# Kernel tuning notes

Measured on AMD Instinct MI355X. Metric: run time of the kernel, lower is better.

## Reference

```python
import jax, jax.numpy as jnp
import numpy as np

# H2RConfig constants
KERNEL = 3
MAX_ROUTES = 1000
STRIDE = 4.0
MIN_SIZE = 32.0
MAX_SIZE = 512.0
SCORE_POWER = 2.0
UNC_WEIGHT = 0.35


def setup_inputs() -> dict:
    key = jax.random.key(0)
    k1, k2, k3 = jax.random.split(key, 3)
    shape = (32, 1, 512, 512)  # [B, 1, H, W] heatmaps at stride 4
    return {
        "route_logits": jax.random.normal(k1, shape, jnp.float32),
        "scale_logits": jax.random.normal(k2, shape, jnp.float32),
        "uncertainty_logits": jax.random.normal(k3, shape, jnp.float32),
        "image_h": 2048,
        "image_w": 2048,
    }


def reference(route_logits, scale_logits, uncertainty_logits, image_h, image_w):
    # score map: sigmoid^power, modulated by uncertainty (use_route_uncertainty=True)
    score = jnp.power(jax.nn.sigmoid(route_logits), SCORE_POWER)
    score = score * (1.0 - UNC_WEIGHT * jax.nn.sigmoid(uncertainty_logits))

    # local-max NMS: 3x3 max pool, stride 1, SAME padding (torch pads with -inf)
    pooled = jax.lax.reduce_window(
        score, -jnp.inf, jax.lax.max,
        window_dimensions=(1, 1, KERNEL, KERNEL),
        window_strides=(1, 1, 1, 1),
        padding="SAME",
    )
    peak_mask = score == pooled
    filtered = jnp.where(peak_mask, score, -1.0)

    B = score.shape[0]
    Wd = score.shape[3]
    flat = filtered.reshape(B, -1)                 # [B, H*W]
    values, indices = jax.lax.top_k(flat, MAX_ROUTES)  # [B, K]
    valid = values > 0.0                            # torch drops these; we mask/pad

    ys = indices // Wd
    xs = indices % Wd
    cx = (xs.astype(jnp.float32) + 0.5) * STRIDE
    cy = (ys.astype(jnp.float32) + 0.5) * STRIDE

    # gather scale / uncertainty at peak locations
    sc = jnp.take_along_axis(scale_logits.reshape(B, -1), indices, axis=1)
    un = jax.nn.sigmoid(jnp.take_along_axis(uncertainty_logits.reshape(B, -1), indices, axis=1))

    side = MIN_SIZE + jax.nn.sigmoid(sc) * (MAX_SIZE - MIN_SIZE)
    side = side * (1.0 + 0.25 * un)
    half = side * 0.5

    iw = float(image_w)
    ih = float(image_h)
    x1 = jnp.clip(cx - half, 0.0, iw - 1.0)
    y1 = jnp.clip(cy - half, 0.0, ih - 1.0)
    x2 = jnp.clip(cx + half, 1.0, iw)
    y2 = jnp.clip(cy + half, 1.0, ih)

    bcol = jnp.broadcast_to(jnp.arange(B, dtype=jnp.float32)[:, None], values.shape)
    rois = jnp.stack([bcol, x1, y1, x2, y2], axis=-1)  # [B, K, 5]

    # padded (fixed-shape) equivalent of torch's variable-length concat
    rois = jnp.where(valid[..., None], rois, 0.0)
    scores = jnp.where(valid, values, 0.0)
    return rois, scores, valid
```

## Files before the change

kernel.cpp:

```cpp
#include <hip/hip_runtime.h>
#include <hip/hip_bf16.h>
#include <math.h>


#define B_   32
#define H_   512
#define W_   512
#define HW_  (H_ * W_)
#define K_   1000
#define ROWS_ 16
#define THR_  512
#define NSTRIP_ 32
#define NBUK_ 4096
#define GCAP_ 2048
#define HSEG_ 128
#define NSEGB_ (NSTRIP_ * 8)
#define HOTBITS_ 0x3F000000u
#define WBASE_ (NBUK_ - 64)
#define FBCAP_ 45056

#define HL_BYTES_  ((size_t)B_ * NSEGB_ * HSEG_ * 8)
#define GW_BYTES_  ((size_t)B_ * NSTRIP_ * 64 * 4)
#define HC_BYTES_  ((size_t)B_ * NSEGB_ * 4)

__device__ __forceinline__ float np_expf(float x) {
#pragma clang fp contract(off)
    const float log2e = 1.44269504088896341f;
    float z = x * log2e;
    float m = rintf(z);
    float r = fmaf(m, -0.693359375f, x);
    r = fmaf(m, 2.12194440e-4f, r);
    float r2 = r * r;
    float p = fmaf(1.9875691500e-4f, r, 1.3981999507e-3f);
    p = fmaf(p, r, 8.3334519073e-3f);
    p = fmaf(p, r, 4.1665795894e-2f);
    p = fmaf(p, r, 1.6666665459e-1f);
    p = fmaf(p, r, 5.0000001201e-1f);
    p = fmaf(p, r2, r);
    p = p + 1.0f;
    int mi = (int)m;
    float sc = __int_as_float((127 + mi) << 23);
    return p * sc;
}

__device__ __forceinline__ float sigmoid_np(float x) {
#pragma clang fp contract(off)
    float e = np_expf(-x);
    float d = 1.0f + e;
    return 1.0f / d;
}

__device__ __forceinline__ float score_ref(float r, float u) {
#pragma clang fp contract(off)
    float s  = sigmoid_np(r);
    float s2 = s * s;
    float su = sigmoid_np(u);
    float t  = 0.35f * su;
    float m  = 1.0f - t;
    return s2 * m;
}

__device__ __forceinline__ float sigmoid_fast(float x) {
    return 1.0f / (1.0f + __expf(-x));
}

__global__ __launch_bounds__(THR_, 4) void fused_peak_kernel(
    const float* __restrict__ route, const float* __restrict__ unc,
    unsigned long long* __restrict__ hotlist,
    unsigned int* __restrict__ ghw,
    int* __restrict__ hcnt8)
{
    __shared__ float sm[ROWS_ + 2][W_];
    __shared__ unsigned int whist[64];

    const int tid   = threadIdx.x;
    const int lane  = tid & 63;
    const int wid   = tid >> 6;
    const int strip = blockIdx.x;
    const int b     = blockIdx.y;
    const int r0    = strip * ROWS_;
    if (tid < 64) whist[tid] = 0u;

    const float4* rb4 = (const float4*)(route + (size_t)b * HW_);
    const float4* ub4 = (const float4*)(unc   + (size_t)b * HW_);
    unsigned long long* hseg =
        hotlist + ((size_t)(b * NSTRIP_ + strip) * 8 + wid) * HSEG_;

    float4 rv[5], uv[5];
    int lrow[5], c4[5]; bool ok[5];
    #pragma unroll
    for (int k = 0; k < 5; ++k) {
        int slot = tid + k * THR_;
        slot = slot < 2303 ? slot : 2303;
        int row = slot >> 7;
        int gy  = r0 - 1 + row;
        lrow[k] = row; c4[k] = slot & 127;
        ok[k]   = (gy >= 0 && gy < H_);
        int cy  = gy < 0 ? 0 : (gy >= H_ ? H_ - 1 : gy);
        rv[k] = rb4[cy * 128 + c4[k]];
        uv[k] = ub4[cy * 128 + c4[k]];
    }
    #pragma unroll
    for (int k = 0; k < 5; ++k) {
        float4 s;
        s.x = score_ref(rv[k].x, uv[k].x);
        s.y = score_ref(rv[k].y, uv[k].y);
        s.z = score_ref(rv[k].z, uv[k].z);
        s.w = score_ref(rv[k].w, uv[k].w);
        if (!ok[k]) { s.x = -INFINITY; s.y = -INFINITY;
                      s.z = -INFINITY; s.w = -INFINITY; }
        *(float4*)&sm[lrow[k]][c4[k] * 4] = s;
    }
    __syncthreads();

    const unsigned long long lt = (1ull << lane) - 1ull;
    int wn = 0;
    #pragma unroll
    for (int j = 0; j < 4; ++j) {
        int g  = tid + j * THR_;
        int ly = 1 + (g >> 7);
        int x0 = (g & 127) * 4;
        int gy = r0 + (ly - 1);
        float4 q0 = *(const float4*)&sm[ly - 1][x0];
        float4 q1 = *(const float4*)&sm[ly    ][x0];
        float4 q2 = *(const float4*)&sm[ly + 1][x0];
        bool hasL = (x0 > 0), hasR = (x0 + 4 < W_);
        float l0 = hasL ? sm[ly - 1][x0 - 1] : -INFINITY;
        float l1 = hasL ? sm[ly    ][x0 - 1] : -INFINITY;
        float l2 = hasL ? sm[ly + 1][x0 - 1] : -INFINITY;
        float e0 = hasR ? sm[ly - 1][x0 + 4] : -INFINITY;
        float e1 = hasR ? sm[ly    ][x0 + 4] : -INFINITY;
        float e2 = hasR ? sm[ly + 1][x0 + 4] : -INFINITY;
        float f_m1 = fmaxf(l0, fmaxf(l1, l2));
        float f_0  = fmaxf(q0.x, fmaxf(q1.x, q2.x));
        float f_1  = fmaxf(q0.y, fmaxf(q1.y, q2.y));
        float f_2  = fmaxf(q0.z, fmaxf(q1.z, q2.z));
        float f_3  = fmaxf(q0.w, fmaxf(q1.w, q2.w));
        float f_4  = fmaxf(e0, fmaxf(e1, e2));
        float tb0  = fmaxf(q0.x, q2.x);
        float tb1  = fmaxf(q0.y, q2.y);
        float tb2  = fmaxf(q0.z, q2.z);
        float tb3  = fmaxf(q0.w, q2.w);
        float vv[4] = { q1.x, q1.y, q1.z, q1.w };
        float mm[4];
        mm[0] = fmaxf(fmaxf(f_m1, f_1), tb0);
        mm[1] = fmaxf(fmaxf(f_0,  f_2), tb1);
        mm[2] = fmaxf(fmaxf(f_1,  f_3), tb2);
        mm[3] = fmaxf(fmaxf(f_2,  f_4), tb3);
        #pragma unroll
        for (int i = 0; i < 4; ++i) {
            bool take = (vv[i] >= mm[i]);
            unsigned int bits = __float_as_uint(vv[i]);
            bool hot = take && (bits >= HOTBITS_);
            unsigned long long hmk = __ballot(hot);
            if (hot) {
                int hp = wn + __popcll(hmk & lt);
                if (hp < HSEG_) {
                    unsigned int idx = (unsigned int)(gy * W_ + x0 + i);
                    hseg[hp] = ((unsigned long long)bits << 32)
                               | (0xFFFFFFFFu - idx);
                    atomicAdd(&whist[(bits >> 18) - WBASE_], 1u);
                }
            }
            wn += __popcll(hmk);
        }
    }
    __syncthreads();

    if (lane == 0)
        hcnt8[(b * NSTRIP_ + strip) * 8 + wid] = wn < HSEG_ ? wn : HSEG_;
    if (tid < 64)
        ghw[(size_t)(b * NSTRIP_ + strip) * 64 + tid] = whist[tid];
}

__global__ __launch_bounds__(1024) void select2_kernel(
    const float* __restrict__ route, const float* __restrict__ unc_r,
    const float* __restrict__ scale, const float* __restrict__ unc,
    const unsigned long long* __restrict__ hotlist,
    const unsigned int* __restrict__ ghw,
    const int* __restrict__ hcnt8,
    unsigned long long* __restrict__ fbbuf,
    const int* __restrict__ ih_p, const int* __restrict__ iw_p,
    float* __restrict__ out)
{
    __shared__ __align__(16) unsigned char u_[(ROWS_ + 2) * W_ * 4];
    __shared__ unsigned int hist[NBUK_];
    __shared__ int sh_T, sh_nc, sh_fb, sh_fn;

    float (*sm)[W_] = (float (*)[W_])u_;
    unsigned int* cursor = (unsigned int*)u_;
    unsigned long long* grp = (unsigned long long*)(u_ + 16384);

    const int b = blockIdx.x, tid = threadIdx.x;
    const int lane = tid & 63, wid = tid >> 6;

    if (tid == 0) { sh_fb = 0; sh_T = 1; sh_nc = 0; sh_fn = 0; }
    if (tid < 64) hist[WBASE_ + tid] = 0u;
    __syncthreads();
    {
        const unsigned int* gw = ghw + (size_t)b * NSTRIP_ * 64;
        for (int i = tid; i < NSTRIP_ * 64; i += 1024) {
            unsigned int v = gw[i];
            if (v) atomicAdd(&hist[WBASE_ + (i & 63)], v);
        }
    }
    __syncthreads();

    if (wid == 0) {
        int cnt = (int)hist[WBASE_ + lane];
        int sum = cnt;
        #pragma unroll
        for (int off = 32; off > 0; off >>= 1)
            sum += __shfl_down(sum, off, 64);
        sum = __shfl(sum, 0, 64);
        if (sum < K_) {
            if (lane == 0) sh_fb = 1;
        } else {
            int suf = cnt;
            #pragma unroll
            for (int off = 1; off < 64; off <<= 1) {
                int o = __shfl_down(suf, off, 64);
                suf += (lane + off < 64) ? o : 0;
            }
            bool cond = suf >= K_;
            unsigned long long mask = __ballot(cond);
            int ls = 63 - __builtin_clzll(mask);
            if (lane >= ls) cursor[WBASE_ + lane] = (unsigned int)(suf - cnt);
            int ncv = __shfl(suf, ls, 64);
            if (lane == 0) { sh_T = WBASE_ + ls; sh_nc = ncv; }
        }
    }
    __syncthreads();
    const int fb = sh_fb;

    if (fb) {
        for (int i = tid; i < NBUK_; i += 1024) hist[i] = 0u;
        __syncthreads();

        const float4* rb4 = (const float4*)(route + (size_t)b * HW_);
        const float4* ub4 = (const float4*)(unc_r + (size_t)b * HW_);
        unsigned long long* fbb = fbbuf + (size_t)b * FBCAP_;

        for (int strip = 0; strip < NSTRIP_; ++strip) {
            const int r0 = strip * ROWS_;
            __syncthreads();
            for (int slot = tid; slot < 2304; slot += 1024) {
                int row = slot >> 7;
                int gy  = r0 - 1 + row;
                int c4  = slot & 127;
                bool okr = (gy >= 0 && gy < H_);
                int cy  = gy < 0 ? 0 : (gy >= H_ ? H_ - 1 : gy);
                float4 r4 = rb4[cy * 128 + c4];
                float4 u4 = ub4[cy * 128 + c4];
                float4 s;
                s.x = score_ref(r4.x, u4.x);
                s.y = score_ref(r4.y, u4.y);
                s.z = score_ref(r4.z, u4.z);
                s.w = score_ref(r4.w, u4.w);
                if (!okr) { s.x = -INFINITY; s.y = -INFINITY;
                            s.z = -INFINITY; s.w = -INFINITY; }
                *(float4*)&sm[row][c4 * 4] = s;
            }
            __syncthreads();
            for (int g = tid; g < 2048; g += 1024) {
                int ly = 1 + (g >> 7);
                int x0 = (g & 127) * 4;
                int gy = r0 + (ly - 1);
                float4 q0 = *(const float4*)&sm[ly - 1][x0];
                float4 q1 = *(const float4*)&sm[ly    ][x0];
                float4 q2 = *(const float4*)&sm[ly + 1][x0];
                bool hasL = (x0 > 0), hasR = (x0 + 4 < W_);
                float l0 = hasL ? sm[ly - 1][x0 - 1] : -INFINITY;
                float l1 = hasL ? sm[ly    ][x0 - 1] : -INFINITY;
                float l2 = hasL ? sm[ly + 1][x0 - 1] : -INFINITY;
                float e0 = hasR ? sm[ly - 1][x0 + 4] : -INFINITY;
                float e1 = hasR ? sm[ly    ][x0 + 4] : -INFINITY;
                float e2 = hasR ? sm[ly + 1][x0 + 4] : -INFINITY;
                float f_m1 = fmaxf(l0, fmaxf(l1, l2));
                float f_0  = fmaxf(q0.x, fmaxf(q1.x, q2.x));
                float f_1  = fmaxf(q0.y, fmaxf(q1.y, q2.y));
                float f_2  = fmaxf(q0.z, fmaxf(q1.z, q2.z));
                float f_3  = fmaxf(q0.w, fmaxf(q1.w, q2.w));
                float f_4  = fmaxf(e0, fmaxf(e1, e2));
                float tb0  = fmaxf(q0.x, q2.x);
                float tb1  = fmaxf(q0.y, q2.y);
                float tb2  = fmaxf(q0.z, q2.z);
                float tb3  = fmaxf(q0.w, q2.w);
                float vv[4] = { q1.x, q1.y, q1.z, q1.w };
                float mm[4];
                mm[0] = fmaxf(fmaxf(f_m1, f_1), tb0);
                mm[1] = fmaxf(fmaxf(f_0,  f_2), tb1);
                mm[2] = fmaxf(fmaxf(f_1,  f_3), tb2);
                mm[3] = fmaxf(fmaxf(f_2,  f_4), tb3);
                #pragma unroll
                for (int i = 0; i < 4; ++i) {
                    if (vv[i] >= mm[i]) {
                        unsigned int bits = __float_as_uint(vv[i]);
                        unsigned int idx  = (unsigned int)(gy * W_ + x0 + i);
                        int p = atomicAdd(&sh_fn, 1);
                        if (p < FBCAP_) {
                            fbb[p] = ((unsigned long long)bits << 32)
                                     | (0xFFFFFFFFu - idx);
                            atomicAdd(&hist[bits >> 18], 1u);
                        }
                    }
                }
            }
        }
        __syncthreads();

        if (wid == 0) {
            int Tv = 0;
            int total = 0;
            for (int c = NBUK_ / 64 - 1; c >= 0; --c) {
                int cnt = (int)hist[c * 64 + lane];
                int sum = cnt;
                #pragma unroll
                for (int off = 32; off > 0; off >>= 1)
                    sum += __shfl_down(sum, off, 64);
                sum = __shfl(sum, 0, 64);
                if (total + sum < K_) { total += sum; continue; }
                int suf = cnt;
                #pragma unroll
                for (int off = 1; off < 64; off <<= 1) {
                    int o = __shfl_down(suf, off, 64);
                    suf += (lane + off < 64) ? o : 0;
                }
                bool cond = (total + suf) >= K_;
                unsigned long long mask = __ballot(cond);
                int ls = 63 - __builtin_clzll(mask);
                Tv = c * 64 + ls;
                break;
            }
            if (Tv < 1) Tv = 1;
            int run = 0;
            for (int cb = NBUK_ - 64; cb >= (Tv & ~63); cb -= 64) {
                int beta = cb + lane;
                int cnt = (beta >= Tv) ? (int)hist[beta] : 0;
                int suf = cnt;
                #pragma unroll
                for (int off = 1; off < 64; off <<= 1) {
                    int o = __shfl_down(suf, off, 64);
                    suf += (lane + off < 64) ? o : 0;
                }
                int chunk_total = __shfl(suf, 0, 64);
                if (beta >= Tv) cursor[beta] = (unsigned int)(run + (suf - cnt));
                run += chunk_total;
            }
            if (lane == 0) { sh_T = Tv; sh_nc = run; }
        }
    }
    __syncthreads();
    const unsigned int T = (unsigned int)sh_T;

    if (!fb) {
        const unsigned long long* hb = hotlist + (size_t)b * NSEGB_ * HSEG_;
        const int* hc = hcnt8 + b * NSEGB_;
        for (int s = wid; s < NSEGB_; s += 16) {
            int c = hc[s];
            const unsigned long long* hs = hb + (size_t)s * HSEG_;
            for (int base = 0; base < c; base += 64) {
                int i = base + lane;
                unsigned long long key = (i < c) ? hs[i] : 0ull;
                unsigned int bk = (unsigned int)(key >> 50);
                if (bk >= T) {
                    unsigned int pos = atomicAdd(&cursor[bk], 1u);
                    if (pos < GCAP_) grp[pos] = key;
                }
            }
        }
    } else {
        const unsigned long long* fbb = fbbuf + (size_t)b * FBCAP_;
        int n = sh_fn; if (n > FBCAP_) n = FBCAP_;
        for (int i = tid; i < n; i += 1024) {
            unsigned long long k = fbb[i];
            unsigned int b0 = (unsigned int)(k >> 50);
            if (b0 >= T) {
                unsigned int pos = atomicAdd(&cursor[b0], 1u);
                if (pos < GCAP_) grp[pos] = k;
            }
        }
    }
    __syncthreads();

    const float fih = (float)(*ih_p);
    const float fiw = (float)(*iw_p);
    float* rois   = out;
    float* scores = out + (size_t)B_ * K_ * 5;
    float* validf = out + (size_t)B_ * K_ * 6;

    int nc = sh_nc;
    int ncEff = nc < GCAP_ ? nc : GCAP_;
    for (int p = tid; p < ncEff; p += 1024) {
        unsigned long long key = grp[p];
        unsigned int beta = (unsigned int)(key >> 50);
        int segEnd   = (int)cursor[beta];
        int segStart = segEnd - (int)hist[beta];
        int qEnd = segEnd < GCAP_ ? segEnd : GCAP_;
        int r = 0;
        for (int q = segStart; q < qEnd; ++q)
            r += (grp[q] > key) ? 1 : 0;
        int rank = segStart + r;
        if (rank < K_) {
            int o = b * K_ + rank;
            unsigned int bits = (unsigned int)(key >> 32);
            float v = __uint_as_float(bits);
            unsigned int idx = 0xFFFFFFFFu - (unsigned int)(key & 0xFFFFFFFFull);
            int y = (int)(idx >> 9), x = (int)(idx & 511u);
            float cx = ((float)x + 0.5f) * 4.0f;
            float cy = ((float)y + 0.5f) * 4.0f;
            float ss = sigmoid_fast(scale[(size_t)b * HW_ + idx]);
            float su = sigmoid_fast(unc  [(size_t)b * HW_ + idx]);
            float side = (32.0f + ss * 480.0f) * (1.0f + 0.25f * su);
            float half = 0.5f * side;
            float x1 = fminf(fmaxf(cx - half, 0.0f), fiw - 1.0f);
            float y1 = fminf(fmaxf(cy - half, 0.0f), fih - 1.0f);
            float x2 = fminf(fmaxf(cx + half, 1.0f), fiw);
            float y2 = fminf(fmaxf(cy + half, 1.0f), fih);
            rois[o * 5 + 0] = (float)b;
            rois[o * 5 + 1] = x1; rois[o * 5 + 2] = y1;
            rois[o * 5 + 3] = x2; rois[o * 5 + 4] = y2;
            scores[o] = v; validf[o] = 1.0f;
        }
    }
    for (int k = nc + tid; k < K_; k += 1024) {
        int o = b * K_ + k;
        rois[o * 5 + 0] = 0.0f; rois[o * 5 + 1] = 0.0f;
        rois[o * 5 + 2] = 0.0f; rois[o * 5 + 3] = 0.0f;
        rois[o * 5 + 4] = 0.0f;
        scores[o] = 0.0f; validf[o] = 0.0f;
    }
}

extern "C" void kernel_launch(void* const* d_in, const int* in_sizes, int n_in,
                              void* d_out, int out_size, void* d_ws, size_t ws_size,
                              hipStream_t stream) {
    const float* route = (const float*)d_in[0];
    const float* scale = (const float*)d_in[1];
    const float* unc   = (const float*)d_in[2];
    const int*   ih    = (const int*)d_in[3];
    const int*   iw    = (const int*)d_in[4];
    float* out = (float*)d_out;

    unsigned char* base = (unsigned char*)d_ws;
    unsigned long long* hotlist = (unsigned long long*)base;
    unsigned int* ghw = (unsigned int*)(base + HL_BYTES_);
    int* hcnt8        = (int*)(base + HL_BYTES_ + GW_BYTES_);
    unsigned long long* fbbuf =
        (unsigned long long*)(base + HL_BYTES_ + GW_BYTES_ + HC_BYTES_);

    dim3 g(NSTRIP_, B_);
    fused_peak_kernel<<<g, THR_, 0, stream>>>(route, unc, hotlist, ghw,
                                              hcnt8);
    select2_kernel<<<B_, 1024, 0, stream>>>(route, unc, scale, unc,
                                            hotlist, ghw, hcnt8, fbbuf,
                                            ih, iw, out);
}
```

Baseline: 172.7 us.

## Move hot-candidate histogram from peak kernel into selection kernel with finer buckets

Drops the per-block shared-memory histogram atomics, the trailing __syncthreads and the ghw global writes from the peak-finding kernel. The selection kernel now builds a finer 2048-bucket histogram (12-bit granularity above the hot threshold) directly from the hotlist entries, then finds the threshold bucket and scatters keys with cursors. This is meant to lighten the bandwidth-bound first kernel and shrink the tie groups in the rank step. The cost is that the single-block-per-batch select kernel reads the hotlist twice and does more work in its threshold scan.

New measurement: 167.6 us. 1.03x faster.

```diff
diff --git a/kernel.cpp b/kernel.cpp
--- a/kernel.cpp
+++ b/kernel.cpp
@@ -12,15 +12,14 @@
 #define THR_  512
 #define NSTRIP_ 32
 #define NBUK_ 4096
+#define NFB_  2048
 #define GCAP_ 2048
 #define HSEG_ 128
 #define NSEGB_ (NSTRIP_ * 8)
 #define HOTBITS_ 0x3F000000u
-#define WBASE_ (NBUK_ - 64)
 #define FBCAP_ 45056
 
 #define HL_BYTES_  ((size_t)B_ * NSEGB_ * HSEG_ * 8)
-#define GW_BYTES_  ((size_t)B_ * NSTRIP_ * 64 * 4)
 #define HC_BYTES_  ((size_t)B_ * NSEGB_ * 4)
 
 __device__ __forceinline__ float np_expf(float x) {
@@ -67,11 +66,9 @@
 __global__ __launch_bounds__(THR_, 4) void fused_peak_kernel(
     const float* __restrict__ route, const float* __restrict__ unc,
     unsigned long long* __restrict__ hotlist,
-    unsigned int* __restrict__ ghw,
     int* __restrict__ hcnt8)
 {
     __shared__ float sm[ROWS_ + 2][W_];
-    __shared__ unsigned int whist[64];
 
     const int tid   = threadIdx.x;
     const int lane  = tid & 63;
@@ -79,7 +76,6 @@
     const int strip = blockIdx.x;
     const int b     = blockIdx.y;
     const int r0    = strip * ROWS_;
-    if (tid < 64) whist[tid] = 0u;
 
     const float4* rb4 = (const float4*)(route + (size_t)b * HW_);
     const float4* ub4 = (const float4*)(unc   + (size_t)b * HW_);
@@ -159,25 +155,19 @@
                     unsigned int idx = (unsigned int)(gy * W_ + x0 + i);
                     hseg[hp] = ((unsigned long long)bits << 32)
                                | (0xFFFFFFFFu - idx);
-                    atomicAdd(&whist[(bits >> 18) - WBASE_], 1u);
                 }
             }
             wn += __popcll(hmk);
         }
     }
-    __syncthreads();
-
     if (lane == 0)
         hcnt8[(b * NSTRIP_ + strip) * 8 + wid] = wn < HSEG_ ? wn : HSEG_;
-    if (tid < 64)
-        ghw[(size_t)(b * NSTRIP_ + strip) * 64 + tid] = whist[tid];
 }
 
 __global__ __launch_bounds__(1024) void select2_kernel(
     const float* __restrict__ route, const float* __restrict__ unc_r,
     const float* __restrict__ scale, const float* __restrict__ unc,
     const unsigned long long* __restrict__ hotlist,
-    const unsigned int* __restrict__ ghw,
     const int* __restrict__ hcnt8,
     unsigned long long* __restrict__ fbbuf,
     const int* __restrict__ ih_p, const int* __restrict__ iw_p,
@@ -185,6 +175,7 @@
 {
     __shared__ __align__(16) unsigned char u_[(ROWS_ + 2) * W_ * 4];
     __shared__ unsigned int hist[NBUK_];
+    __shared__ int segc[NSEGB_];
     __shared__ int sh_T, sh_nc, sh_fb, sh_fn;
 
     float (*sm)[W_] = (float (*)[W_])u_;
@@ -194,49 +185,154 @@
     const int b = blockIdx.x, tid = threadIdx.x;
     const int lane = tid & 63, wid = tid >> 6;
 
-    if (tid == 0) { sh_fb = 0; sh_T = 1; sh_nc = 0; sh_fn = 0; }
-    if (tid < 64) hist[WBASE_ + tid] = 0u;
+    if (tid == 0) { sh_fb = 0; sh_T = 0; sh_nc = 0; sh_fn = 0; }
+    for (int i = tid; i < NSEGB_; i += 1024) segc[i] = hcnt8[b * NSEGB_ + i];
+    for (int i = tid; i < NFB_; i += 1024) hist[i] = 0u;
     __syncthreads();
-    {
-        const unsigned int* gw = ghw + (size_t)b * NSTRIP_ * 64;
-        for (int i = tid; i < NSTRIP_ * 64; i += 1024) {
-            unsigned int v = gw[i];
-            if (v) atomicAdd(&hist[WBASE_ + (i & 63)], v);
-        }
-    }
-    __syncthreads();
-
     if (wid == 0) {
-        int cnt = (int)hist[WBASE_ + lane];
-        int sum = cnt;
+        int t = 0;
+        for (int i = lane; i < NSEGB_; i += 64) t += segc[i];
         #pragma unroll
         for (int off = 32; off > 0; off >>= 1)
-            sum += __shfl_down(sum, off, 64);
-        sum = __shfl(sum, 0, 64);
-        if (sum < K_) {
-            if (lane == 0) sh_fb = 1;
-        } else {
-            int suf = cnt;
-            #pragma unroll
-            for (int off = 1; off < 64; off <<= 1) {
-                int o = __shfl_down(suf, off, 64);
-                suf += (lane + off < 64) ? o : 0;
-            }
-            bool cond = suf >= K_;
-            unsigned long long mask = __ballot(cond);
-            int ls = 63 - __builtin_clzll(mask);
-            if (lane >= ls) cursor[WBASE_ + lane] = (unsigned int)(suf - cnt);
-            int ncv = __shfl(suf, ls, 64);
-            if (lane == 0) { sh_T = WBASE_ + ls; sh_nc = ncv; }
-        }
+            t += __shfl_down(t, off, 64);
+        if (lane == 0 && t < K_) sh_fb = 1;
     }
     __syncthreads();
     const int fb = sh_fb;
 
-    if (fb) {
-        for (int i = tid; i < NBUK_; i += 1024) hist[i] = 0u;
+    if (!fb) {
+        const unsigned long long* hb = hotlist + (size_t)b * NSEGB_ * HSEG_;
+
+        for (int s = wid; s < NSEGB_; s += 16) {
+            int c = segc[s];
+            const unsigned long long* hs = hb + (size_t)s * HSEG_;
+            for (int base = 0; base < c; base += 64) {
+                int i = base + lane;
+                if (i < c) {
+                    unsigned int bits = (unsigned int)(hs[i] >> 32);
+                    unsigned int fbk = (bits - HOTBITS_) >> 12;
+                    if (fbk > NFB_ - 1) fbk = NFB_ - 1;
+                    atomicAdd(&hist[fbk], 1u);
+                }
+            }
+        }
         __syncthreads();
 
+        if (wid == 0) {
+            int Tv = 0;
+            int total = 0;
+            for (int c = NFB_ / 64 - 1; c >= 0; --c) {
+                int cnt = (int)hist[c * 64 + lane];
+                int sum = cnt;
+                #pragma unroll
+                for (int off = 32; off > 0; off >>= 1)
+                    sum += __shfl_down(sum, off, 64);
+                sum = __shfl(sum, 0, 64);
+                if (total + sum < K_) { total += sum; continue; }
+                int suf = cnt;
+                #pragma unroll
+                for (int off = 1; off < 64; off <<= 1) {
+                    int o = __shfl_down(suf, off, 64);
+                    suf += (lane + off < 64) ? o : 0;
+                }
+                bool cond = (total + suf) >= K_;
+                unsigned long long mask = __ballot(cond);
+                int ls = 63 - __builtin_clzll(mask);
+                Tv = c * 64 + ls;
+                break;
+            }
+            int run = 0;
+            for (int cb = NFB_ - 64; cb >= (Tv & ~63); cb -= 64) {
+                int beta = cb + lane;
+                int cnt = (beta >= Tv) ? (int)hist[beta] : 0;
+                int suf = cnt;
+                #pragma unroll
+                for (int off = 1; off < 64; off <<= 1) {
+                    int o = __shfl_down(suf, off, 64);
+                    suf += (lane + off < 64) ? o : 0;
+                }
+                int chunk_total = __shfl(suf, 0, 64);
+                if (beta >= Tv) cursor[beta] = (unsigned int)(run + (suf - cnt));
+                run += chunk_total;
+            }
+            if (lane == 0) { sh_T = Tv; sh_nc = run; }
+        }
+        __syncthreads();
+
+        const unsigned int T = (unsigned int)sh_T;
+        for (int s = wid; s < NSEGB_; s += 16) {
+            int c = segc[s];
+            const unsigned long long* hs = hb + (size_t)s * HSEG_;
+            for (int base = 0; base < c; base += 64) {
+                int i = base + lane;
+                if (i < c) {
+                    unsigned long long key = hs[i];
+                    unsigned int bits = (unsigned int)(key >> 32);
+                    unsigned int fbk = (bits - HOTBITS_) >> 12;
+                    if (fbk > NFB_ - 1) fbk = NFB_ - 1;
+                    if (fbk >= T) {
+                        unsigned int pos = atomicAdd(&cursor[fbk], 1u);
+                        if (pos < GCAP_) grp[pos] = key;
+                    }
+                }
+            }
+        }
+        __syncthreads();
+
+        const float fih = (float)(*ih_p);
+        const float fiw = (float)(*iw_p);
+        float* rois   = out;
+        float* scores = out + (size_t)B_ * K_ * 5;
+        float* validf = out + (size_t)B_ * K_ * 6;
+
+        int nc = sh_nc;
+        int ncEff = nc < GCAP_ ? nc : GCAP_;
+        for (int p = tid; p < ncEff; p += 1024) {
+            unsigned long long key = grp[p];
+            unsigned int bits = (unsigned int)(key >> 32);
+            unsigned int beta = (bits - HOTBITS_) >> 12;
+            if (beta > NFB_ - 1) beta = NFB_ - 1;
+            int segEnd   = (int)cursor[beta];
+            int segStart = segEnd - (int)hist[beta];
+            int qEnd = segEnd < GCAP_ ? segEnd : GCAP_;
+            int r = 0;
+            for (int q = segStart; q < qEnd; ++q)
+                r += (grp[q] > key) ? 1 : 0;
+            int rank = segStart + r;
+            if (rank < K_) {
+                int o = b * K_ + rank;
+                float v = __uint_as_float(bits);
+                unsigned int idx = 0xFFFFFFFFu - (unsigned int)(key & 0xFFFFFFFFull);
+                int y = (int)(idx >> 9), x = (int)(idx & 511u);
+                float cx = ((float)x + 0.5f) * 4.0f;
+                float cy = ((float)y + 0.5f) * 4.0f;
+                float ss = sigmoid_fast(scale[(size_t)b * HW_ + idx]);
+                float su = sigmoid_fast(unc  [(size_t)b * HW_ + idx]);
+                float side = (32.0f + ss * 480.0f) * (1.0f + 0.25f * su);
+                float half = 0.5f * side;
+                float x1 = fminf(fmaxf(cx - half, 0.0f), fiw - 1.0f);
+                float y1 = fminf(fmaxf(cy - half, 0.0f), fih - 1.0f);
+                float x2 = fminf(fmaxf(cx + half, 1.0f), fiw);
+                float y2 = fminf(fmaxf(cy + half, 1.0f), fih);
+                rois[o * 5 + 0] = (float)b;
+                rois[o * 5 + 1] = x1; rois[o * 5 + 2] = y1;
+                rois[o * 5 + 3] = x2; rois[o * 5 + 4] = y2;
+                scores[o] = v; validf[o] = 1.0f;
+            }
+        }
+        for (int k = sh_nc + tid; k < K_; k += 1024) {
+            int o = b * K_ + k;
+            rois[o * 5 + 0] = 0.0f; rois[o * 5 + 1] = 0.0f;
+            rois[o * 5 + 2] = 0.0f; rois[o * 5 + 3] = 0.0f;
+            rois[o * 5 + 4] = 0.0f;
+            scores[o] = 0.0f; validf[o] = 0.0f;
+        }
+        return;
+    }
+
+    for (int i = tid; i < NBUK_; i += 1024) hist[i] = 0u;
+    __syncthreads();
+    {
         const float4* rb4 = (const float4*)(route + (size_t)b * HW_);
         const float4* ub4 = (const float4*)(unc_r + (size_t)b * HW_);
         unsigned long long* fbb = fbbuf + (size_t)b * FBCAP_;
@@ -349,86 +445,68 @@
             }
             if (lane == 0) { sh_T = Tv; sh_nc = run; }
         }
-    }
-    __syncthreads();
-    const unsigned int T = (unsigned int)sh_T;
-
-    if (!fb) {
-        const unsigned long long* hb = hotlist + (size_t)b * NSEGB_ * HSEG_;
-        const int* hc = hcnt8 + b * NSEGB_;
-        for (int s = wid; s < NSEGB_; s += 16) {
-            int c = hc[s];
-            const unsigned long long* hs = hb + (size_t)s * HSEG_;
-            for (int base = 0; base < c; base += 64) {
-                int i = base + lane;
-                unsigned long long key = (i < c) ? hs[i] : 0ull;
-                unsigned int bk = (unsigned int)(key >> 50);
-                if (bk >= T) {
-                    unsigned int pos = atomicAdd(&cursor[bk], 1u);
-                    if (pos < GCAP_) grp[pos] = key;
-                }
-            }
-        }
-    } else {
-        const unsigned long long* fbb = fbbuf + (size_t)b * FBCAP_;
+        __syncthreads();
+
+        const unsigned int T = (unsigned int)sh_T;
+        const unsigned long long* fbbr = fbbuf + (size_t)b * FBCAP_;
         int n = sh_fn; if (n > FBCAP_) n = FBCAP_;
         for (int i = tid; i < n; i += 1024) {
-            unsigned long long k = fbb[i];
+            unsigned long long k = fbbr[i];
             unsigned int b0 = (unsigned int)(k >> 50);
             if (b0 >= T) {
                 unsigned int pos = atomicAdd(&cursor[b0], 1u);
                 if (pos < GCAP_) grp[pos] = k;
             }
         }
-    }
-    __syncthreads();
-
-    const float fih = (float)(*ih_p);
-    const float fiw = (float)(*iw_p);
-    float* rois   = out;
-    float* scores = out + (size_t)B_ * K_ * 5;
-    float* validf = out + (size_t)B_ * K_ * 6;
-
-    int nc = sh_nc;
-    int ncEff = nc < GCAP_ ? nc : GCAP_;
-    for (int p = tid; p < ncEff; p += 1024) {
-        unsigned long long key = grp[p];
-        unsigned int beta = (unsigned int)(key >> 50);
-        int segEnd   = (int)cursor[beta];
-        int segStart = segEnd - (int)hist[beta];
-        int qEnd = segEnd < GCAP_ ? segEnd : GCAP_;
-        int r = 0;
-        for (int q = segStart; q < qEnd; ++q)
-            r += (grp[q] > key) ? 1 : 0;
-        int rank = segStart + r;
-        if (rank < K_) {
-            int o = b * K_ + rank;
-            unsigned int bits = (unsigned int)(key >> 32);
-            float v = __uint_as_float(bits);
-            unsigned int idx = 0xFFFFFFFFu - (unsigned int)(key & 0xFFFFFFFFull);
-            int y = (int)(idx >> 9), x = (int)(idx & 511u);
-            float cx = ((float)x + 0.5f) * 4.0f;
-            float cy = ((float)y + 0.5f) * 4.0f;
-            float ss = sigmoid_fast(scale[(size_t)b * HW_ + idx]);
-            float su = sigmoid_fast(unc  [(size_t)b * HW_ + idx]);
-            float side = (32.0f + ss * 480.0f) * (1.0f + 0.25f * su);
-            float half = 0.5f * side;
-            float x1 = fminf(fmaxf(cx - half, 0.0f), fiw - 1.0f);
-            float y1 = fminf(fmaxf(cy - half, 0.0f), fih - 1.0f);
-            float x2 = fminf(fmaxf(cx + half, 1.0f), fiw);
-            float y2 = fminf(fmaxf(cy + half, 1.0f), fih);
-            rois[o * 5 + 0] = (float)b;
-            rois[o * 5 + 1] = x1; rois[o * 5 + 2] = y1;
-            rois[o * 5 + 3] = x2; rois[o * 5 + 4] = y2;
-            scores[o] = v; validf[o] = 1.0f;
-        }
-    }
-    for (int k = nc + tid; k < K_; k += 1024) {
-        int o = b * K_ + k;
-        rois[o * 5 + 0] = 0.0f; rois[o * 5 + 1] = 0.0f;
-        rois[o * 5 + 2] = 0.0f; rois[o * 5 + 3] = 0.0f;
-        rois[o * 5 + 4] = 0.0f;
-        scores[o] = 0.0f; validf[o] = 0.0f;
+        __syncthreads();
+
+        const float fih = (float)(*ih_p);
+        const float fiw = (float)(*iw_p);
+        float* rois   = out;
+        float* scores = out + (size_t)B_ * K_ * 5;
+        float* validf = out + (size_t)B_ * K_ * 6;
+
+        int nc = sh_nc;
+        int ncEff = nc < GCAP_ ? nc : GCAP_;
+        for (int p = tid; p < ncEff; p += 1024) {
+            unsigned long long key = grp[p];
+            unsigned int beta = (unsigned int)(key >> 50);
+            int segEnd   = (int)cursor[beta];
+            int segStart = segEnd - (int)hist[beta];
+            int qEnd = segEnd < GCAP_ ? segEnd : GCAP_;
+            int r = 0;
+            for (int q = segStart; q < qEnd; ++q)
+                r += (grp[q] > key) ? 1 : 0;
+            int rank = segStart + r;
+            if (rank < K_) {
+                int o = b * K_ + rank;
+                unsigned int bits = (unsigned int)(key >> 32);
+                float v = __uint_as_float(bits);
+                unsigned int idx = 0xFFFFFFFFu - (unsigned int)(key & 0xFFFFFFFFull);
+                int y = (int)(idx >> 9), x = (int)(idx & 511u);
+                float cx = ((float)x + 0.5f) * 4.0f;
+                float cy = ((float)y + 0.5f) * 4.0f;
+                float ss = sigmoid_fast(scale[(size_t)b * HW_ + idx]);
+                float su = sigmoid_fast(unc  [(size_t)b * HW_ + idx]);
+                float side = (32.0f + ss * 480.0f) * (1.0f + 0.25f * su);
+                float half = 0.5f * side;
+                float x1 = fminf(fmaxf(cx - half, 0.0f), fiw - 1.0f);
+                float y1 = fminf(fmaxf(cy - half, 0.0f), fih - 1.0f);
+                float x2 = fminf(fmaxf(cx + half, 1.0f), fiw);
+                float y2 = fminf(fmaxf(cy + half, 1.0f), fih);
+                rois[o * 5 + 0] = (float)b;
+                rois[o * 5 + 1] = x1; rois[o * 5 + 2] = y1;
+                rois[o * 5 + 3] = x2; rois[o * 5 + 4] = y2;
+                scores[o] = v; validf[o] = 1.0f;
+            }
+        }
+        for (int k = sh_nc + tid; k < K_; k += 1024) {
+            int o = b * K_ + k;
+            rois[o * 5 + 0] = 0.0f; rois[o * 5 + 1] = 0.0f;
+            rois[o * 5 + 2] = 0.0f; rois[o * 5 + 3] = 0.0f;
+            rois[o * 5 + 4] = 0.0f;
+            scores[o] = 0.0f; validf[o] = 0.0f;
+        }
     }
 }
 
@@ -444,15 +522,13 @@
 
     unsigned char* base = (unsigned char*)d_ws;
     unsigned long long* hotlist = (unsigned long long*)base;
-    unsigned int* ghw = (unsigned int*)(base + HL_BYTES_);
-    int* hcnt8        = (int*)(base + HL_BYTES_ + GW_BYTES_);
+    int* hcnt8        = (int*)(base + HL_BYTES_);
     unsigned long long* fbbuf =
-        (unsigned long long*)(base + HL_BYTES_ + GW_BYTES_ + HC_BYTES_);
+        (unsigned long long*)(base + HL_BYTES_ + HC_BYTES_);
 
     dim3 g(NSTRIP_, B_);
-    fused_peak_kernel<<<g, THR_, 0, stream>>>(route, unc, hotlist, ghw,
-                                              hcnt8);
+    fused_peak_kernel<<<g, THR_, 0, stream>>>(route, unc, hotlist, hcnt8);
     select2_kernel<<<B_, 1024, 0, stream>>>(route, unc, scale, unc,
-                                            hotlist, ghw, hcnt8, fbbuf,
+                                            hotlist, hcnt8, fbbuf,
                                             ih, iw, out);
 }
```
